# Kernel tuning notes

Measured on AMD Instinct MI355X. Metric: run time of the kernel, lower is better.

## Reference

```python
import jax, jax.numpy as jnp
import numpy as np

D_EMB = 64
N_HEADS = 8
D_K = D_EMB // N_HEADS


def setup_inputs() -> dict:
    key = jax.random.key(0)
    ks = jax.random.split(key, 7)
    B, N = 4, 512
    s = 0.02
    return {
        "n": jax.random.normal(ks[0], (B, N, D_EMB), jnp.float32),
        "e": jax.random.normal(ks[1], (B, N, N, D_EMB), jnp.float32),
        # weights stored as (in, out); torch Linear applies x @ W.T
        "W_qkv": jax.random.normal(ks[2], (D_EMB, 3 * D_EMB), jnp.float32) * s,
        "O_n": jax.random.normal(ks[3], (D_EMB, D_EMB), jnp.float32) * s,
        "W_g": jax.random.normal(ks[4], (D_EMB, N_HEADS), jnp.float32) * s,
        "W_e": jax.random.normal(ks[5], (D_EMB, N_HEADS), jnp.float32) * s,
        "O_e": jax.random.normal(ks[6], (N_HEADS, D_EMB), jnp.float32) * s,
    }


def reference(n, e, W_qkv, O_n, W_g, W_e, O_e):
    B, N, _ = n.shape
    H, dk = N_HEADS, D_K
    # QKV projection -> [B, H, N, dk] each
    qkv = (n @ W_qkv).reshape(B, N, 3, H, dk)
    Q = jnp.transpose(qkv[:, :, 0], (0, 2, 1, 3))
    K = jnp.transpose(qkv[:, :, 1], (0, 2, 1, 3))
    V = jnp.transpose(qkv[:, :, 2], (0, 2, 1, 3))
    # per-head edge bias E and gate G: [B, H, N, N]
    E = jnp.transpose(e @ W_e, (0, 3, 1, 2))
    G = jax.nn.sigmoid(jnp.transpose(e @ W_g, (0, 3, 1, 2)))
    dynamic_centrality = jnp.log1p(G.sum(-1))  # [B, H, N]
    # scaled, clamped attention scores plus edge bias
    A_raw = jnp.einsum("bhnd,bhmd->bhnm", Q, K) * (dk ** -0.5)
    A_raw = jnp.clip(A_raw, -5.0, 5.0)
    _E = A_raw + E  # pre-softmax scores, reused for edge output
    A = jax.nn.softmax(_E, axis=-1)
    _V = jnp.einsum("bhnm,bhmd->bhnd", A, V)
    _V = _V * dynamic_centrality[..., None]  # centrality rescale
    n_out = jnp.transpose(_V, (0, 2, 1, 3)).reshape(B, N, H * dk) @ O_n
    e_out = jnp.transpose(_E, (0, 2, 3, 1)) @ O_e  # [B, N, N, d_emb]
    return (n_out, e_out)
```

## Files before the change

### kernel.cpp

```cpp
#include <hip/hip_runtime.h>

#define NN 512
#define SCALE 0.35355339059327373f
#define SMAX 6.0f

typedef short bf16x8 __attribute__((ext_vector_type(8)));
typedef float f32x4 __attribute__((ext_vector_type(4)));

static __device__ __forceinline__ unsigned short bhi16(float x) {
    return (unsigned short)(__float_as_uint(x) >> 16);
}

__global__ __launch_bounds__(64) void qkv_proj(const float* __restrict__ nin,
                                               const float* __restrict__ Wqkv,
                                               float* __restrict__ qkv,
                                               unsigned short* __restrict__ kbf) {
    const int r = blockIdx.x;
    const int j = threadIdx.x;
    const float* nr = nin + (size_t)r * 64;
    float a0 = 0.f, a1 = 0.f, a2 = 0.f;
#pragma unroll
    for (int d = 0; d < 64; ++d) {
        const float nv = nr[d];
        const float* wr = Wqkv + d * 192;
        a0 = fmaf(nv, wr[j], a0);
        a1 = fmaf(nv, wr[64 + j], a1);
        a2 = fmaf(nv, wr[128 + j], a2);
    }
    float* o = qkv + (size_t)r * 192;
    o[j] = a0; o[64 + j] = a1; o[128 + j] = a2;
    kbf[(size_t)r * 64 + j] = bhi16(a1);
}

__device__ __forceinline__ void gload16f(const float* g, float* l) {
    __builtin_amdgcn_global_load_lds(
        (const __attribute__((address_space(1))) unsigned int*)(g),
        (__attribute__((address_space(3))) unsigned int*)(l), 16, 0, 0);
}
__device__ __forceinline__ void gload16u(const unsigned short* g, unsigned short* l) {
    __builtin_amdgcn_global_load_lds(
        (const __attribute__((address_space(1))) unsigned int*)(g),
        (__attribute__((address_space(3))) unsigned int*)(l), 16, 0, 0);
}
#define WAITV(N) asm volatile("s_waitcnt vmcnt(" #N ")" ::: "memory")
#define BARRIER() __builtin_amdgcn_s_barrier()

__global__ __launch_bounds__(256, 5) void edge_mfma7(
    const float* __restrict__ e,
    const float* __restrict__ qkv,
    const unsigned short* __restrict__ kbf,
    const float* __restrict__ We,
    const float* __restrict__ Wg,
    const float* __restrict__ Oe,
    float* __restrict__ e_out,
    float* __restrict__ pvw,
    float* __restrict__ dngs)
{
    __shared__ float ebuf[4][16][64];
    __shared__ unsigned short kbl[4][16][64];
    __shared__ float uni[1088];
    __shared__ float Oelds[512];
    __shared__ float red[256];
    __shared__ float wdn[4][8], wgs[4][8];

    float* const Wl = uni;
    float* const Qlds = uni + 1024;
    auto E_lds = reinterpret_cast<float(*)[32][8]>(uni);

    const int t = threadIdx.x, w = t >> 6, l = t & 63;
    const int a2 = l >> 4, m16 = l & 15;
    const int bid = blockIdx.x;
    const int wg = (bid & 7) * 1024 + (bid >> 3);
    const int bn = wg >> 2, chunk = wg & 3;
    const int b = bn >> 9;
    const int rowc = chunk * 128 + w * 32;
    const float* __restrict__ Qp = qkv + (size_t)bn * 192;
    const float* __restrict__ ebase = e + (size_t)bn * 32768;
    float* __restrict__ eob = e_out + (size_t)bn * 32768;

#define STAGE_E(s) do {                                                          \
        _Pragma("unroll")                                                        \
        for (int i_ = 0; i_ < 4; ++i_) {                                         \
            const int lrow = i_ * 4 + (l >> 4);                                  \
            gload16f(ebase + (size_t)(rowc + (s) * 16 + lrow) * 64 + (((l & 15) ^ lrow) * 4), \
                     &ebuf[w][i_ * 4][0]);                                       \
        } } while (0)
#define STAGE_K(s) do {                                                          \
        _Pragma("unroll")                                                        \
        for (int i_ = 0; i_ < 2; ++i_) {                                         \
            const int r8 = i_ * 8 + (l >> 3);                                    \
            gload16u(kbf + (size_t)(b * NN + rowc + (s) * 16 + r8) * 64 + (((l & 7) ^ (r8 & 7)) * 8), \
                     &kbl[w][i_ * 8][0]);                                        \
        } } while (0)

    {
        const float* wsrc = (w < 2) ? (We + w * 256) : (Wg + (w - 2) * 256);
        gload16f(wsrc + l * 4, &Wl[w * 256]);
        if (l < 16) gload16f(Qp + l * 4, &Qlds[0]);
        if (l < 32) gload16f(Oe + w * 128 + l * 4, &Oelds[w * 128]);
    }
    STAGE_E(0); STAGE_K(0);

    WAITV(6);
    BARRIER();

    const int colbase = (m16 < 8) ? m16 : (504 + m16);
    bf16x8 WB[2], QdB[2];
#pragma unroll
    for (int c = 0; c < 2; ++c) {
        const int head = c * 4 + a2;
#pragma unroll
        for (int j = 0; j < 8; ++j) {
            const int d = c * 32 + a2 * 8 + j;
            WB[c][j] = (short)bhi16(Wl[d * 8 + colbase]);
            QdB[c][j] = (m16 == head) ? (short)bhi16(Qlds[d]) : (short)0;
        }
    }
    float dn = 0.f, gs = 0.f;
    BARRIER();

#define SLAB(s) do {                                                             \
        f32x4 c1 = {0.f, 0.f, 0.f, 0.f}, c2 = {0.f, 0.f, 0.f, 0.f};             \
        _Pragma("unroll")                                                        \
        for (int c = 0; c < 2; ++c) {                                            \
            const int g0 = c * 8 + a2 * 2;                                       \
            const float4 e0 = *(const float4*)&ebuf[w][m16][((g0 ^ m16) * 4)];   \
            const float4 e1 = *(const float4*)&ebuf[w][m16][(((g0 + 1) ^ m16) * 4)]; \
            bf16x8 ac;                                                           \
            ac[0] = (short)bhi16(e0.x); ac[1] = (short)bhi16(e0.y);              \
            ac[2] = (short)bhi16(e0.z); ac[3] = (short)bhi16(e0.w);              \
            ac[4] = (short)bhi16(e1.x); ac[5] = (short)bhi16(e1.y);              \
            ac[6] = (short)bhi16(e1.z); ac[7] = (short)bhi16(e1.w);              \
            c1 = __builtin_amdgcn_mfma_f32_16x16x32_bf16(ac, WB[c], c1, 0, 0, 0); \
            const bf16x8 kf = *(const bf16x8*)&kbl[w][m16]                       \
                                  [(((c * 4 + a2) ^ (m16 & 7)) * 8)];            \
            c2 = __builtin_amdgcn_mfma_f32_16x16x32_bf16(kf, QdB[c], c2, 0, 0, 0); \
        }                                                                        \
        if (m16 < 8) {                                                           \
            _Pragma("unroll")                                                    \
            for (int r = 0; r < 4; ++r) {                                        \
                const float E_ = fminf(fmaxf(c2[r] * SCALE, -5.f), 5.f) + c1[r]; \
                dn += __expf(E_ - SMAX);                                         \
                E_lds[w][(s) * 16 + a2 * 4 + r][m16] = E_;                       \
            }                                                                    \
        } else {                                                                 \
            _Pragma("unroll")                                                    \
            for (int r = 0; r < 4; ++r) gs += 1.f / (1.f + __expf(-c1[r]));      \
        } } while (0)

    WAITV(0);
    SLAB(0);
    STAGE_E(1); STAGE_K(1);
    WAITV(0);
    SLAB(1);

    dn += __shfl_xor(dn, 16, 64); dn += __shfl_xor(dn, 32, 64);
    gs += __shfl_xor(gs, 16, 64); gs += __shfl_xor(gs, 32, 64);
    if (a2 == 0 && m16 < 8) wdn[w][m16] = dn;
    if (a2 == 0 && m16 >= 8) wgs[w][m16 - 8] = gs;

    {
        const int k = l & 7, hh = (l >> 3) & 7;
        const float* vb = qkv + (size_t)(b * NN + rowc) * 192 + 128 + hh * 8 + k;
        float acc = 0.f;
#pragma unroll 8
        for (int i = 0; i < 32; ++i) {
            const float p = __expf(E_lds[w][i][hh] - SMAX);
            acc = fmaf(p, vb[(size_t)i * 192], acc);
        }
        red[t] = acc;
    }
    __syncthreads();
    if (t < 64)
        pvw[(size_t)wg * 64 + t] = red[t] + red[64 + t] + red[128 + t] + red[192 + t];
    if (t < 8)
        dngs[(size_t)wg * 16 + t] = wdn[0][t] + wdn[1][t] + wdn[2][t] + wdn[3][t];
    else if (t < 16)
        dngs[(size_t)wg * 16 + t] = wgs[0][t - 8] + wgs[1][t - 8] + wgs[2][t - 8] + wgs[3][t - 8];

    {
        const int j4 = l & 15, mr = l >> 4;
        float oc[8][4];
#pragma unroll
        for (int h = 0; h < 8; ++h) {
            const float4 v = *(const float4*)&Oelds[h * 64 + j4 * 4];
            oc[h][0] = v.x; oc[h][1] = v.y; oc[h][2] = v.z; oc[h][3] = v.w;
        }
#pragma unroll 2
        for (int p = 0; p < 8; ++p) {
            const int mloc = p * 4 + mr;
            const float* er = &E_lds[w][mloc][0];
            const float4 ra = *reinterpret_cast<const float4*>(er);
            const float4 rb = *reinterpret_cast<const float4*>(er + 4);
            float o0 = ra.x * oc[0][0], o1 = ra.x * oc[0][1], o2 = ra.x * oc[0][2], o3 = ra.x * oc[0][3];
            o0 = fmaf(ra.y, oc[1][0], o0); o1 = fmaf(ra.y, oc[1][1], o1); o2 = fmaf(ra.y, oc[1][2], o2); o3 = fmaf(ra.y, oc[1][3], o3);
            o0 = fmaf(ra.z, oc[2][0], o0); o1 = fmaf(ra.z, oc[2][1], o1); o2 = fmaf(ra.z, oc[2][2], o2); o3 = fmaf(ra.z, oc[2][3], o3);
            o0 = fmaf(ra.w, oc[3][0], o0); o1 = fmaf(ra.w, oc[3][1], o1); o2 = fmaf(ra.w, oc[3][2], o2); o3 = fmaf(ra.w, oc[3][3], o3);
            o0 = fmaf(rb.x, oc[4][0], o0); o1 = fmaf(rb.x, oc[4][1], o1); o2 = fmaf(rb.x, oc[4][2], o2); o3 = fmaf(rb.x, oc[4][3], o3);
            o0 = fmaf(rb.y, oc[5][0], o0); o1 = fmaf(rb.y, oc[5][1], o1); o2 = fmaf(rb.y, oc[5][2], o2); o3 = fmaf(rb.y, oc[5][3], o3);
            o0 = fmaf(rb.z, oc[6][0], o0); o1 = fmaf(rb.z, oc[6][1], o1); o2 = fmaf(rb.z, oc[6][2], o2); o3 = fmaf(rb.z, oc[6][3], o3);
            o0 = fmaf(rb.w, oc[7][0], o0); o1 = fmaf(rb.w, oc[7][1], o1); o2 = fmaf(rb.w, oc[7][2], o2); o3 = fmaf(rb.w, oc[7][3], o3);
            reinterpret_cast<float4*>(eob + (size_t)(rowc + mloc) * 64 + j4 * 4)[0]
                = make_float4(o0, o1, o2, o3);
        }
    }
#undef STAGE_E
#undef STAGE_K
#undef SLAB
}

__global__ __launch_bounds__(64) void nout_fin(
    const float* __restrict__ pvw,
    const float* __restrict__ dngs,
    const float* __restrict__ On,
    float* __restrict__ n_out)
{
    __shared__ float vfin[64];
    const int bn = blockIdx.x, t = threadIdx.x;
    const int hh = t >> 3;
    float pv = 0.f, den = 0.f, gsum = 0.f;
#pragma unroll
    for (int c = 0; c < 4; ++c) {
        const size_t wg = (size_t)bn * 4 + c;
        pv += pvw[wg * 64 + t];
        den += dngs[wg * 16 + hh];
        gsum += dngs[wg * 16 + 8 + hh];
    }
    vfin[t] = pv * (1.f / den) * log1pf(gsum);
    __syncthreads();
    float acc = 0.f;
#pragma unroll
    for (int i = 0; i < 64; ++i)
        acc = fmaf(vfin[i], On[i * 64 + t], acc);
    n_out[(size_t)bn * 64 + t] = acc;
}

extern "C" void kernel_launch(void* const* d_in, const int* in_sizes, int n_in,
                              void* d_out, int out_size, void* d_ws, size_t ws_size,
                              hipStream_t stream) {
    const float* n_in_p = (const float*)d_in[0];
    const float* e_p    = (const float*)d_in[1];
    const float* Wqkv   = (const float*)d_in[2];
    const float* On     = (const float*)d_in[3];
    const float* Wg     = (const float*)d_in[4];
    const float* We     = (const float*)d_in[5];
    const float* Oe     = (const float*)d_in[6];
    float* out = (float*)d_out;
    float* n_out = out;
    float* e_out = out + (size_t)4 * 512 * 64;
    float* qkv = (float*)d_ws;
    float* pvw = qkv + 393216;
    float* dngs = pvw + 524288;
    unsigned short* kbf = (unsigned short*)(dngs + 131072);

    hipLaunchKernelGGL(qkv_proj, dim3(4 * NN), dim3(64), 0, stream, n_in_p, Wqkv, qkv, kbf);
    hipLaunchKernelGGL(edge_mfma7, dim3(8192), dim3(256), 0, stream,
                       e_p, qkv, kbf, We, Wg, Oe, e_out, pvw, dngs);
    hipLaunchKernelGGL(nout_fin, dim3(4 * NN), dim3(64), 0, stream,
                       pvw, dngs, On, n_out);
}
```

Baseline: 154.2 us.

## Load K fragments directly to registers and cache softmax numerators in LDS

```diff
diff --git a/kernel.cpp b/kernel.cpp
--- a/kernel.cpp
+++ b/kernel.cpp
@@ -9,6 +9,9 @@
 
 static __device__ __forceinline__ unsigned short bhi16(float x) {
     return (unsigned short)(__float_as_uint(x) >> 16);
+}
+static __device__ __forceinline__ float bf2f(unsigned short u) {
+    return __uint_as_float(((unsigned int)u) << 16);
 }
 
 __global__ __launch_bounds__(64) void qkv_proj(const float* __restrict__ nin,
@@ -37,15 +40,10 @@
         (const __attribute__((address_space(1))) unsigned int*)(g),
         (__attribute__((address_space(3))) unsigned int*)(l), 16, 0, 0);
 }
-__device__ __forceinline__ void gload16u(const unsigned short* g, unsigned short* l) {
-    __builtin_amdgcn_global_load_lds(
-        (const __attribute__((address_space(1))) unsigned int*)(g),
-        (__attribute__((address_space(3))) unsigned int*)(l), 16, 0, 0);
-}
 #define WAITV(N) asm volatile("s_waitcnt vmcnt(" #N ")" ::: "memory")
 #define BARRIER() __builtin_amdgcn_s_barrier()
 
-__global__ __launch_bounds__(256, 5) void edge_mfma7(
+__global__ __launch_bounds__(256, 6) void edge_mfma8(
     const float* __restrict__ e,
     const float* __restrict__ qkv,
     const unsigned short* __restrict__ kbf,
@@ -57,8 +55,8 @@
     float* __restrict__ dngs)
 {
     __shared__ float ebuf[4][16][64];
-    __shared__ unsigned short kbl[4][16][64];
     __shared__ float uni[1088];
+    __shared__ unsigned short Pl[4][32][8];
     __shared__ float Oelds[512];
     __shared__ float red[256];
     __shared__ float wdn[4][8], wgs[4][8];
@@ -85,13 +83,6 @@
             gload16f(ebase + (size_t)(rowc + (s) * 16 + lrow) * 64 + (((l & 15) ^ lrow) * 4), \
                      &ebuf[w][i_ * 4][0]);                                       \
         } } while (0)
-#define STAGE_K(s) do {                                                          \
-        _Pragma("unroll")                                                        \
-        for (int i_ = 0; i_ < 2; ++i_) {                                         \
-            const int r8 = i_ * 8 + (l >> 3);                                    \
-            gload16u(kbf + (size_t)(b * NN + rowc + (s) * 16 + r8) * 64 + (((l & 7) ^ (r8 & 7)) * 8), \
-                     &kbl[w][i_ * 8][0]);                                        \
-        } } while (0)
 
     {
         const float* wsrc = (w < 2) ? (We + w * 256) : (Wg + (w - 2) * 256);
@@ -99,19 +90,27 @@
         if (l < 16) gload16f(Qp + l * 4, &Qlds[0]);
         if (l < 32) gload16f(Oe + w * 128 + l * 4, &Oelds[w * 128]);
     }
-    STAGE_E(0); STAGE_K(0);
-
-    WAITV(6);
+    STAGE_E(0);
+    bf16x8 kr0[2], kr1[2];
+    {
+        const unsigned short* kb0 = kbf + (size_t)(b * NN + rowc + m16) * 64 + a2 * 16;
+        kr0[0] = *(const bf16x8*)(kb0);
+        kr0[1] = *(const bf16x8*)(kb0 + 8);
+        kr1[0] = *(const bf16x8*)(kb0 + 1024);
+        kr1[1] = *(const bf16x8*)(kb0 + 1032);
+    }
+
+    WAITV(8);
     BARRIER();
 
     const int colbase = (m16 < 8) ? m16 : (504 + m16);
     bf16x8 WB[2], QdB[2];
 #pragma unroll
     for (int c = 0; c < 2; ++c) {
-        const int head = c * 4 + a2;
+        const int head = a2 * 2 + c;
 #pragma unroll
         for (int j = 0; j < 8; ++j) {
-            const int d = c * 32 + a2 * 8 + j;
+            const int d = a2 * 16 + c * 8 + j;
             WB[c][j] = (short)bhi16(Wl[d * 8 + colbase]);
             QdB[c][j] = (m16 == head) ? (short)bhi16(Qlds[d]) : (short)0;
         }
@@ -119,11 +118,11 @@
     float dn = 0.f, gs = 0.f;
     BARRIER();
 
-#define SLAB(s) do {                                                             \
+#define SLAB(s, KR) do {                                                         \
         f32x4 c1 = {0.f, 0.f, 0.f, 0.f}, c2 = {0.f, 0.f, 0.f, 0.f};             \
         _Pragma("unroll")                                                        \
         for (int c = 0; c < 2; ++c) {                                            \
-            const int g0 = c * 8 + a2 * 2;                                       \
+            const int g0 = a2 * 4 + c * 2;                                       \
             const float4 e0 = *(const float4*)&ebuf[w][m16][((g0 ^ m16) * 4)];   \
             const float4 e1 = *(const float4*)&ebuf[w][m16][(((g0 + 1) ^ m16) * 4)]; \
             bf16x8 ac;                                                           \
@@ -132,27 +131,27 @@
             ac[4] = (short)bhi16(e1.x); ac[5] = (short)bhi16(e1.y);              \
             ac[6] = (short)bhi16(e1.z); ac[7] = (short)bhi16(e1.w);              \
             c1 = __builtin_amdgcn_mfma_f32_16x16x32_bf16(ac, WB[c], c1, 0, 0, 0); \
-            const bf16x8 kf = *(const bf16x8*)&kbl[w][m16]                       \
-                                  [(((c * 4 + a2) ^ (m16 & 7)) * 8)];            \
-            c2 = __builtin_amdgcn_mfma_f32_16x16x32_bf16(kf, QdB[c], c2, 0, 0, 0); \
+            c2 = __builtin_amdgcn_mfma_f32_16x16x32_bf16(KR[c], QdB[c], c2, 0, 0, 0); \
         }                                                                        \
         if (m16 < 8) {                                                           \
             _Pragma("unroll")                                                    \
             for (int r = 0; r < 4; ++r) {                                        \
                 const float E_ = fminf(fmaxf(c2[r] * SCALE, -5.f), 5.f) + c1[r]; \
-                dn += __expf(E_ - SMAX);                                         \
+                const float P_ = __expf(E_ - SMAX);                              \
+                dn += P_;                                                        \
                 E_lds[w][(s) * 16 + a2 * 4 + r][m16] = E_;                       \
+                Pl[w][(s) * 16 + a2 * 4 + r][m16] = bhi16(P_);                   \
             }                                                                    \
         } else {                                                                 \
             _Pragma("unroll")                                                    \
             for (int r = 0; r < 4; ++r) gs += 1.f / (1.f + __expf(-c1[r]));      \
         } } while (0)
 
+    WAITV(4);
+    SLAB(0, kr0);
+    STAGE_E(1);
     WAITV(0);
-    SLAB(0);
-    STAGE_E(1); STAGE_K(1);
-    WAITV(0);
-    SLAB(1);
+    SLAB(1, kr1);
 
     dn += __shfl_xor(dn, 16, 64); dn += __shfl_xor(dn, 32, 64);
     gs += __shfl_xor(gs, 16, 64); gs += __shfl_xor(gs, 32, 64);
@@ -165,8 +164,7 @@
         float acc = 0.f;
 #pragma unroll 8
         for (int i = 0; i < 32; ++i) {
-            const float p = __expf(E_lds[w][i][hh] - SMAX);
-            acc = fmaf(p, vb[(size_t)i * 192], acc);
+            acc = fmaf(bf2f(Pl[w][i][hh]), vb[(size_t)i * 192], acc);
         }
         red[t] = acc;
     }
@@ -205,7 +203,6 @@
         }
     }
 #undef STAGE_E
-#undef STAGE_K
 #undef SLAB
 }
 
@@ -254,7 +251,7 @@
     unsigned short* kbf = (unsigned short*)(dngs + 131072);
 
     hipLaunchKernelGGL(qkv_proj, dim3(4 * NN), dim3(64), 0, stream, n_in_p, Wqkv, qkv, kbf);
-    hipLaunchKernelGGL(edge_mfma7, dim3(8192), dim3(256), 0, stream,
+    hipLaunchKernelGGL(edge_mfma8, dim3(8192), dim3(256), 0, stream,
                        e_p, qkv, kbf, We, Wg, Oe, e_out, pvw, dngs);
     hipLaunchKernelGGL(nout_fin, dim3(4 * NN), dim3(64), 0, stream,
                        pvw, dngs, On, n_out);
```

Measured after the change: 468.7 us. 204% more time.
